# Optimization experiments

Hardware: AMD Instinct MI355X
Metric: run time of the kernel (lower is better)

## Reference

```python
import jax, jax.numpy as jnp
import numpy as np

N_NODES = 10000
N_EDGES = 640000
D = 128


def _sage_conv(x, src, dst, W_l, b, W_r):
    # PyG SAGEConv (mean aggr): out = lin_l(mean_{j in N(i)} x_j) + lin_r(x_i)
    msgs = x[src]                                        # [E, D_in] gather
    agg = jax.ops.segment_sum(msgs, dst, num_segments=N_NODES)  # [N, D_in]
    deg = jax.ops.segment_sum(jnp.ones((src.shape[0],), x.dtype), dst,
                              num_segments=N_NODES)
    agg = agg / jnp.maximum(deg, 1.0)[:, None]           # mean; isolated nodes -> 0
    return agg @ W_l + b + x @ W_r


def setup_inputs() -> dict:
    key = jax.random.key(0)
    ks = jax.random.split(key, 8)
    s = 1.0 / np.sqrt(D)
    return {
        "x": jax.random.normal(ks[0], (N_NODES, D), dtype=jnp.float32),
        "edge_index": jax.random.randint(ks[1], (2, N_EDGES), 0, N_NODES, dtype=jnp.int64),
        "W_l0": jax.random.normal(ks[2], (D, D), dtype=jnp.float32) * s,
        "b0": jnp.zeros((D,), dtype=jnp.float32),
        "W_r0": jax.random.normal(ks[3], (D, D), dtype=jnp.float32) * s,
        "W_l1": jax.random.normal(ks[4], (D, D), dtype=jnp.float32) * s,
        "b1": jnp.zeros((D,), dtype=jnp.float32),
        "W_r1": jax.random.normal(ks[5], (D, D), dtype=jnp.float32) * s,
    }


def reference(x, edge_index, W_l0, b0, W_r0, W_l1, b1, W_r1):
    # Dropout(p=0.3) is identity in eval mode (reference runs inference math).
    src, dst = edge_index[0], edge_index[1]
    h = jax.nn.elu(_sage_conv(x, src, dst, W_l0, b0, W_r0))
    h = jax.nn.elu(_sage_conv(h, src, dst, W_l1, b1, W_r1))
    return h
```

## Files before the change

kernel.cpp:

```cpp
#include <hip/hip_runtime.h>

#define N_NODES 10000
#define N_EDGES 640000
#define D 128
#define MAXDEG 128
#define NBUCK 157
#define BCAP 6144
#define EPT 10

typedef unsigned int uint;
typedef unsigned short u16;
typedef short bf16x8 __attribute__((ext_vector_type(8)));
typedef float f32x4 __attribute__((ext_vector_type(4)));

__device__ __forceinline__ u16 f2bf(float f) {
    uint u = __float_as_uint(f);
    return (u16)((u + 0x7fffu + ((u >> 16) & 1u)) >> 16);
}
__device__ __forceinline__ float bflo(uint v) { return __uint_as_float(v << 16); }
__device__ __forceinline__ float bfhi(uint v) { return __uint_as_float(v & 0xffff0000u); }

__global__ void detect_kernel(const void* ei, int* flag) {
    const int* p = (const int*)ei;
    bool nz = false;
    for (int it = 0; it < 16; ++it) {
        int i = 2 * (threadIdx.x + it * 256) + 1;
        if (p[i] != 0) nz = true;
    }
    if (__any(nz) && (threadIdx.x & 63) == 0) flag[0] = 1;
}

__device__ __forceinline__ int edge_at(const void* ei, int is32, int idx) {
    if (is32) return ((const int*)ei)[idx];
    return (int)((const long long*)ei)[idx];
}

__global__ __launch_bounds__(256)
void binp1_kernel(const void* __restrict__ ei, const int* __restrict__ flag,
                  int* __restrict__ gcount, uint* __restrict__ gbucket) {
    __shared__ int hist[NBUCK];
    __shared__ int base[NBUCK];
    const int t = threadIdx.x;
    if (t < NBUCK) hist[t] = 0;
    __syncthreads();
    const int is32 = *flag;
    const int e0 = blockIdx.x * (256 * EPT);
    uint pk[EPT];
    int  rk[EPT];
#pragma unroll
    for (int i = 0; i < EPT; ++i) {
        int e  = e0 + i * 256 + t;
        int s  = edge_at(ei, is32, e);
        int dn = edge_at(ei, is32, N_EDGES + e);
        pk[i] = ((uint)dn << 16) | (uint)s;
        rk[i] = atomicAdd(&hist[dn >> 6], 1);
    }
    __syncthreads();
    if (t < NBUCK) base[t] = atomicAdd(&gcount[t], hist[t]);
    __syncthreads();
#pragma unroll
    for (int i = 0; i < EPT; ++i) {
        int bkt = (int)(pk[i] >> 22);
        int pos = base[bkt] + rk[i];
        if (pos < BCAP) gbucket[(size_t)bkt * BCAP + pos] = pk[i];
    }
}

__global__ __launch_bounds__(256)
void binp2_kernel(const int* __restrict__ gcount, const uint* __restrict__ gbucket,
                  u16* __restrict__ adj, int* __restrict__ deg_g) {
    __shared__ __align__(16) u16 tile[64][MAXDEG];
    __shared__ int cur[64];
    const int b = blockIdx.x;
    const int t = threadIdx.x;
    if (t < 64) cur[t] = 0;
    __syncthreads();
    const int total = min(gcount[b], BCAP);
    for (int e = t; e < total; e += 256) {
        uint pk = gbucket[(size_t)b * BCAP + e];
        int ln  = (int)((pk >> 16) & 63u);
        int src = (int)(pk & 0xffffu);
        int r = atomicAdd(&cur[ln], 1);
        if (r < MAXDEG) tile[ln][r] = (u16)src;
    }
    __syncthreads();
    const int node0 = b * 64;
    if (t < 64 && node0 + t < N_NODES) deg_g[node0 + t] = cur[t];
    const uint4* ts = (const uint4*)&tile[0][0];
#pragma unroll
    for (int q = 0; q < 4; ++q) {
        int i = t + q * 256;
        int node = node0 + (i >> 4);
        if (node < N_NODES) ((uint4*)(adj + (size_t)node * MAXDEG))[i & 15] = ts[i];
    }
}

__global__ void cast_kernel(const float* __restrict__ in, uint* __restrict__ outb) {
    int t = blockIdx.x * 256 + threadIdx.x;
    if (t >= N_NODES * D / 8) return;
    const float4* p = (const float4*)in + (size_t)t * 2;
    float4 a = p[0], b = p[1];
    uint4 r;
    r.x = (uint)f2bf(a.x) | ((uint)f2bf(a.y) << 16);
    r.y = (uint)f2bf(a.z) | ((uint)f2bf(a.w) << 16);
    r.z = (uint)f2bf(b.x) | ((uint)f2bf(b.y) << 16);
    r.w = (uint)f2bf(b.z) | ((uint)f2bf(b.w) << 16);
    ((uint4*)outb)[t] = r;
}

__global__ __launch_bounds__(256)
void wprep_kernel(const float* __restrict__ Wl0, const float* __restrict__ Wr0,
                  const float* __restrict__ Wl1, const float* __restrict__ Wr1,
                  u16* __restrict__ WT0, u16* __restrict__ WT1) {
    const int b = blockIdx.x;
    const int layer = b >> 7, d = b & 127, k = threadIdx.x;
    const float* Wl = layer ? Wl1 : Wl0;
    const float* Wr = layer ? Wr1 : Wr0;
    u16* WT = layer ? WT1 : WT0;
    float v = (k < 128) ? Wl[k * D + d] : Wr[(k - 128) * D + d];
    WT[(size_t)d * 256 + k] = f2bf(v);
}

__global__ __launch_bounds__(256)
void gather_kernel(const uint* __restrict__ xb2, const u16* __restrict__ adj,
                   const int* __restrict__ deg_g, uint* __restrict__ aggb2) {
    const int node = blockIdx.x * 4 + (threadIdx.x >> 6);
    const int lane = threadIdx.x & 63;
    const int dg = deg_g[node];
    const int cnt = min(dg, MAXDEG);
    const uint* __restrict__ rowu = (const uint*)(adj + (size_t)node * MAXDEG);
    float a0 = 0.f, a1 = 0.f;
    const int nb16 = cnt >> 4;
    if (nb16 > 0) {
        uint pkb[8];
#pragma unroll
        for (int i = 0; i < 8; ++i) pkb[i] = rowu[i];
        for (int b = 0; b < nb16; ++b) {
            uint cur[8];
#pragma unroll
            for (int i = 0; i < 8; ++i) cur[i] = pkb[i];
            if (b + 1 < nb16) {
#pragma unroll
                for (int i = 0; i < 8; ++i) pkb[i] = rowu[(b + 1) * 8 + i];
            }
            uint v[16];
#pragma unroll
            for (int i = 0; i < 8; ++i) {
                v[2 * i]     = xb2[(size_t)(cur[i] & 0xffffu) * 64 + lane];
                v[2 * i + 1] = xb2[(size_t)(cur[i] >> 16)     * 64 + lane];
            }
#pragma unroll
            for (int i = 0; i < 16; ++i) { a0 += bflo(v[i]); a1 += bfhi(v[i]); }
        }
    }
    for (int p = nb16 << 4; p < cnt; ++p) {
        uint v = xb2[(size_t)((const u16*)rowu)[p] * 64 + lane];
        a0 += bflo(v);
        a1 += bfhi(v);
    }
    float inv = 1.0f / fmaxf((float)dg, 1.0f);
    aggb2[(size_t)node * 64 + lane] = (uint)f2bf(a0 * inv) | ((uint)f2bf(a1 * inv) << 16);
}

__global__ __launch_bounds__(256)
void mfma_gemm_kernel(const uint* __restrict__ aggb2, const uint* __restrict__ xb2,
                      const u16* __restrict__ WT, const float* __restrict__ bias,
                      float* __restrict__ outf ,
                      u16* __restrict__ outb ) {
    __shared__ __align__(16) u16 A_lds[16 * 256];
    const int t = threadIdx.x;
    const int nb = blockIdx.x * 16;
    {
        const int row = t >> 4, c = t & 15;
        const int node = nb + row;
        uint4 va = ((const uint4*)(aggb2 + (size_t)node * 64))[c];
        uint4 vx = ((const uint4*)(xb2  + (size_t)node * 64))[c];
        char* base = (char*)A_lds + row * 512;
        const int swz = (row & 7) << 4;
        *(uint4*)(base + ((c * 16) ^ swz))       = va;
        *(uint4*)(base + ((256 + c * 16) ^ swz)) = vx;
    }
    __syncthreads();

    const int w = t >> 6, l = t & 63;
    const int lr = l & 15, g = l >> 4;
    f32x4 acc0 = {0.f, 0.f, 0.f, 0.f}, acc1 = {0.f, 0.f, 0.f, 0.f};
    const char* abase = (const char*)A_lds + lr * 512;
    const int aswz = (lr & 7) << 4;
    const u16* wt0 = WT + (size_t)(w * 32 + lr) * 256;
    const u16* wt1 = WT + (size_t)(w * 32 + 16 + lr) * 256;
#pragma unroll
    for (int kk = 0; kk < 8; ++kk) {
        bf16x8 af  = *(const bf16x8*)(abase + ((kk * 64 + g * 16) ^ aswz));
        bf16x8 bf0 = *(const bf16x8*)(wt0 + kk * 32 + g * 8);
        bf16x8 bf1 = *(const bf16x8*)(wt1 + kk * 32 + g * 8);
        acc0 = __builtin_amdgcn_mfma_f32_16x16x32_bf16(af, bf0, acc0, 0, 0, 0);
        acc1 = __builtin_amdgcn_mfma_f32_16x16x32_bf16(af, bf1, acc1, 0, 0, 0);
    }

    const int col0 = w * 32 + lr, col1 = col0 + 16;
    const float b0v = bias[col0], b1v = bias[col1];
#pragma unroll
    for (int j = 0; j < 4; ++j) {
        const int node = nb + g * 4 + j;
        float v0 = acc0[j] + b0v; v0 = v0 > 0.f ? v0 : expm1f(v0);
        float v1 = acc1[j] + b1v; v1 = v1 > 0.f ? v1 : expm1f(v1);
        if (outf) {
            outf[(size_t)node * D + col0] = v0;
            outf[(size_t)node * D + col1] = v1;
        }
        if (outb) {
            outb[(size_t)node * D + col0] = f2bf(v0);
            outb[(size_t)node * D + col1] = f2bf(v1);
        }
    }
}

extern "C" void kernel_launch(void* const* d_in, const int* in_sizes, int n_in,
                              void* d_out, int out_size, void* d_ws, size_t ws_size,
                              hipStream_t stream) {
    const float* x   = (const float*)d_in[0];
    const void*  ei  = d_in[1];
    const float* Wl0 = (const float*)d_in[2];
    const float* b0  = (const float*)d_in[3];
    const float* Wr0 = (const float*)d_in[4];
    const float* Wl1 = (const float*)d_in[5];
    const float* b1  = (const float*)d_in[6];
    const float* Wr1 = (const float*)d_in[7];
    float* out = (float*)d_out;

    char* ws = (char*)d_ws;
    int*  flag    = (int*)(ws + 0);
    int*  gcount  = (int*)(ws + 1024);
    int*  deg     = (int*)(ws + 4096);
    u16*  adj     = (u16*)(ws + 65536);
    uint* gbucket = (uint*)(ws + 3145728);
    uint* xb2     = (uint*)(ws + 3145728);
    uint* yb2     = (uint*)(ws + 5767168);
    uint* aggb2   = (uint*)(ws + 8388608);
    u16*  WT0     = (u16*)(ws + 11010048);
    u16*  WT1     = (u16*)(ws + 11075584);

    hipMemsetAsync(ws, 0, 2048, stream);

    detect_kernel<<<1, 256, 0, stream>>>(ei, flag);
    binp1_kernel<<<250, 256, 0, stream>>>(ei, flag, gcount, gbucket);
    binp2_kernel<<<NBUCK, 256, 0, stream>>>(gcount, gbucket, adj, deg);
    cast_kernel<<<625, 256, 0, stream>>>(x, xb2);
    wprep_kernel<<<256, 256, 0, stream>>>(Wl0, Wr0, Wl1, Wr1, WT0, WT1);

    gather_kernel<<<2500, 256, 0, stream>>>(xb2, adj, deg, aggb2);
    mfma_gemm_kernel<<<625, 256, 0, stream>>>(aggb2, xb2, WT0, b0, (float*)0, (u16*)yb2);

    gather_kernel<<<2500, 256, 0, stream>>>(yb2, adj, deg, aggb2);
    mfma_gemm_kernel<<<625, 256, 0, stream>>>(aggb2, yb2, WT1, b1, out, (u16*)0);
}
```

Measured before the change: 85.97 us.

## Vectorize neighbor gather with zero-row padding and merge preprocessing launches

The gather kernel now splits each wave into four 16-lane groups. Each group loads a full 256-byte neighbor row with uint4 loads, so four neighbors are processed at once, and the partial sums are combined with cross-lane shuffles. Adjacency rows are padded with a dedicated zero row (ZROW), zeroed in both the x and y buffers, which removes the scalar tail loop. The separate detect, binning-phase-2, cast and weight-prep launches are folded: index-width detection moves into each binp1 block, and the other three stages become one multi-role prep kernel. This cuts launch count and gives wider memory transactions, at the cost of reading padded entries, extra shuffles, and relying on per-block width detection.

```diff
diff --git a/kernel.cpp b/kernel.cpp
--- a/kernel.cpp
+++ b/kernel.cpp
@@ -6,7 +6,8 @@
 #define MAXDEG 128
 #define NBUCK 157
 #define BCAP 6144
-#define EPT 10
+#define EPT 5
+#define ZROW 10000
 
 typedef unsigned int uint;
 typedef unsigned short u16;
@@ -20,31 +21,25 @@
 __device__ __forceinline__ float bflo(uint v) { return __uint_as_float(v << 16); }
 __device__ __forceinline__ float bfhi(uint v) { return __uint_as_float(v & 0xffff0000u); }
 
-__global__ void detect_kernel(const void* ei, int* flag) {
-    const int* p = (const int*)ei;
-    bool nz = false;
-    for (int it = 0; it < 16; ++it) {
-        int i = 2 * (threadIdx.x + it * 256) + 1;
-        if (p[i] != 0) nz = true;
-    }
-    if (__any(nz) && (threadIdx.x & 63) == 0) flag[0] = 1;
-}
-
 __device__ __forceinline__ int edge_at(const void* ei, int is32, int idx) {
     if (is32) return ((const int*)ei)[idx];
     return (int)((const long long*)ei)[idx];
 }
 
 __global__ __launch_bounds__(256)
-void binp1_kernel(const void* __restrict__ ei, const int* __restrict__ flag,
-                  int* __restrict__ gcount, uint* __restrict__ gbucket) {
+void binp1_kernel(const void* __restrict__ ei, int* __restrict__ gcount,
+                  uint* __restrict__ gbucket) {
     __shared__ int hist[NBUCK];
     __shared__ int base[NBUCK];
+    __shared__ int s_is32;
     const int t = threadIdx.x;
     if (t < NBUCK) hist[t] = 0;
-    __syncthreads();
-    const int is32 = *flag;
+    if (t == 0) s_is32 = 0;
+    __syncthreads();
     const int e0 = blockIdx.x * (256 * EPT);
+    if (((const int*)ei)[2 * (e0 + t) + 1] != 0) s_is32 = 1;
+    __syncthreads();
+    const int is32 = s_is32;
     uint pk[EPT];
     int  rk[EPT];
 #pragma unroll
@@ -67,99 +62,119 @@
 }
 
 __global__ __launch_bounds__(256)
-void binp2_kernel(const int* __restrict__ gcount, const uint* __restrict__ gbucket,
-                  u16* __restrict__ adj, int* __restrict__ deg_g) {
+void prep_kernel(const int* __restrict__ gcount, const uint* __restrict__ gbucket,
+                 u16* __restrict__ adj, int* __restrict__ deg_g,
+                 const float* __restrict__ x, uint* __restrict__ xb2,
+                 const float* __restrict__ Wl0, const float* __restrict__ Wr0,
+                 const float* __restrict__ Wl1, const float* __restrict__ Wr1,
+                 u16* __restrict__ WT0, u16* __restrict__ WT1) {
+    const int b = blockIdx.x;
+    const int t = threadIdx.x;
     __shared__ __align__(16) u16 tile[64][MAXDEG];
     __shared__ int cur[64];
-    const int b = blockIdx.x;
-    const int t = threadIdx.x;
-    if (t < 64) cur[t] = 0;
-    __syncthreads();
-    const int total = min(gcount[b], BCAP);
-    for (int e = t; e < total; e += 256) {
-        uint pk = gbucket[(size_t)b * BCAP + e];
-        int ln  = (int)((pk >> 16) & 63u);
-        int src = (int)(pk & 0xffffu);
-        int r = atomicAdd(&cur[ln], 1);
-        if (r < MAXDEG) tile[ln][r] = (u16)src;
-    }
-    __syncthreads();
-    const int node0 = b * 64;
-    if (t < 64 && node0 + t < N_NODES) deg_g[node0 + t] = cur[t];
-    const uint4* ts = (const uint4*)&tile[0][0];
-#pragma unroll
-    for (int q = 0; q < 4; ++q) {
-        int i = t + q * 256;
-        int node = node0 + (i >> 4);
-        if (node < N_NODES) ((uint4*)(adj + (size_t)node * MAXDEG))[i & 15] = ts[i];
-    }
-}
-
-__global__ void cast_kernel(const float* __restrict__ in, uint* __restrict__ outb) {
-    int t = blockIdx.x * 256 + threadIdx.x;
-    if (t >= N_NODES * D / 8) return;
-    const float4* p = (const float4*)in + (size_t)t * 2;
-    float4 a = p[0], b = p[1];
-    uint4 r;
-    r.x = (uint)f2bf(a.x) | ((uint)f2bf(a.y) << 16);
-    r.y = (uint)f2bf(a.z) | ((uint)f2bf(a.w) << 16);
-    r.z = (uint)f2bf(b.x) | ((uint)f2bf(b.y) << 16);
-    r.w = (uint)f2bf(b.z) | ((uint)f2bf(b.w) << 16);
-    ((uint4*)outb)[t] = r;
-}
-
-__global__ __launch_bounds__(256)
-void wprep_kernel(const float* __restrict__ Wl0, const float* __restrict__ Wr0,
-                  const float* __restrict__ Wl1, const float* __restrict__ Wr1,
-                  u16* __restrict__ WT0, u16* __restrict__ WT1) {
-    const int b = blockIdx.x;
-    const int layer = b >> 7, d = b & 127, k = threadIdx.x;
-    const float* Wl = layer ? Wl1 : Wl0;
-    const float* Wr = layer ? Wr1 : Wr0;
-    u16* WT = layer ? WT1 : WT0;
-    float v = (k < 128) ? Wl[k * D + d] : Wr[(k - 128) * D + d];
-    WT[(size_t)d * 256 + k] = f2bf(v);
+    if (b < NBUCK) {
+        uint* tw = (uint*)&tile[0][0];
+#pragma unroll
+        for (int q = 0; q < 16; ++q) tw[t + q * 256] = ((uint)ZROW << 16) | ZROW;
+        if (t < 64) cur[t] = 0;
+        __syncthreads();
+        const int total = min(gcount[b], BCAP);
+        for (int e = t; e < total; e += 256) {
+            uint pk = gbucket[(size_t)b * BCAP + e];
+            int ln = (int)((pk >> 16) & 63u);
+            int r = atomicAdd(&cur[ln], 1);
+            if (r < MAXDEG) tile[ln][r] = (u16)(pk & 0xffffu);
+        }
+        __syncthreads();
+        const int node0 = b * 64;
+        if (t < 64 && node0 + t < N_NODES) deg_g[node0 + t] = cur[t];
+        const uint4* ts = (const uint4*)&tile[0][0];
+#pragma unroll
+        for (int q = 0; q < 4; ++q) {
+            int i = t + q * 256;
+            int node = node0 + (i >> 4);
+            if (node < N_NODES) ((uint4*)(adj + (size_t)node * MAXDEG))[i & 15] = ts[i];
+        }
+    } else if (b < NBUCK + 625) {
+        int idx = (b - NBUCK) * 256 + t;
+        const float4* p = (const float4*)x + (size_t)idx * 2;
+        float4 a = p[0], bb = p[1];
+        uint4 r;
+        r.x = (uint)f2bf(a.x) | ((uint)f2bf(a.y) << 16);
+        r.y = (uint)f2bf(a.z) | ((uint)f2bf(a.w) << 16);
+        r.z = (uint)f2bf(bb.x) | ((uint)f2bf(bb.y) << 16);
+        r.w = (uint)f2bf(bb.z) | ((uint)f2bf(bb.w) << 16);
+        ((uint4*)xb2)[idx] = r;
+    } else if (b < NBUCK + 625 + 256) {
+        int b2 = b - (NBUCK + 625);
+        int layer = b2 >> 7, d = b2 & 127, k = t;
+        const float* Wl = layer ? Wl1 : Wl0;
+        const float* Wr = layer ? Wr1 : Wr0;
+        u16* WT = layer ? WT1 : WT0;
+        float v = (k < 128) ? Wl[k * D + d] : Wr[(k - 128) * D + d];
+        WT[(size_t)d * 256 + k] = f2bf(v);
+    } else {
+        if (t < 16) ((uint4*)(xb2 + (size_t)ZROW * 64))[t] = make_uint4(0, 0, 0, 0);
+    }
 }
 
 __global__ __launch_bounds__(256)
 void gather_kernel(const uint* __restrict__ xb2, const u16* __restrict__ adj,
                    const int* __restrict__ deg_g, uint* __restrict__ aggb2) {
     const int node = blockIdx.x * 4 + (threadIdx.x >> 6);
-    const int lane = threadIdx.x & 63;
+    const int l = threadIdx.x & 63;
+    const int g = l >> 4;
+    const int c = l & 15;
+    const int half = g >> 1;
+    const int sh = (g & 1) << 4;
     const int dg = deg_g[node];
     const int cnt = min(dg, MAXDEG);
-    const uint* __restrict__ rowu = (const uint*)(adj + (size_t)node * MAXDEG);
-    float a0 = 0.f, a1 = 0.f;
-    const int nb16 = cnt >> 4;
-    if (nb16 > 0) {
-        uint pkb[8];
-#pragma unroll
-        for (int i = 0; i < 8; ++i) pkb[i] = rowu[i];
-        for (int b = 0; b < nb16; ++b) {
-            uint cur[8];
-#pragma unroll
-            for (int i = 0; i < 8; ++i) cur[i] = pkb[i];
-            if (b + 1 < nb16) {
-#pragma unroll
-                for (int i = 0; i < 8; ++i) pkb[i] = rowu[(b + 1) * 8 + i];
-            }
-            uint v[16];
-#pragma unroll
-            for (int i = 0; i < 8; ++i) {
-                v[2 * i]     = xb2[(size_t)(cur[i] & 0xffffu) * 64 + lane];
-                v[2 * i + 1] = xb2[(size_t)(cur[i] >> 16)     * 64 + lane];
-            }
-#pragma unroll
-            for (int i = 0; i < 16; ++i) { a0 += bflo(v[i]); a1 += bfhi(v[i]); }
-        }
-    }
-    for (int p = nb16 << 4; p < cnt; ++p) {
-        uint v = xb2[(size_t)((const u16*)rowu)[p] * 64 + lane];
-        a0 += bflo(v);
-        a1 += bfhi(v);
-    }
-    float inv = 1.0f / fmaxf((float)dg, 1.0f);
-    aggb2[(size_t)node * 64 + lane] = (uint)f2bf(a0 * inv) | ((uint)f2bf(a1 * inv) << 16);
+    const uint4* __restrict__ rowq = (const uint4*)(adj + (size_t)node * MAXDEG);
+    float acc[8];
+#pragma unroll
+    for (int i = 0; i < 8; ++i) acc[i] = 0.f;
+    const int nch = (cnt + 15) >> 4;
+#pragma unroll 2
+    for (int ch = 0; ch < nch; ++ch) {
+        uint4 wa = rowq[2 * ch];
+        uint4 wb = rowq[2 * ch + 1];
+        uint a0 = half ? wa.y : wa.x;
+        uint a1 = half ? wa.w : wa.z;
+        uint b0 = half ? wb.y : wb.x;
+        uint b1 = half ? wb.w : wb.z;
+        uint id0 = (a0 >> sh) & 0xffffu;
+        uint id1 = (a1 >> sh) & 0xffffu;
+        uint id2 = (b0 >> sh) & 0xffffu;
+        uint id3 = (b1 >> sh) & 0xffffu;
+        uint4 v0 = ((const uint4*)(xb2 + (size_t)id0 * 64))[c];
+        uint4 v1 = ((const uint4*)(xb2 + (size_t)id1 * 64))[c];
+        uint4 v2 = ((const uint4*)(xb2 + (size_t)id2 * 64))[c];
+        uint4 v3 = ((const uint4*)(xb2 + (size_t)id3 * 64))[c];
+        acc[0] += bflo(v0.x) + bflo(v1.x) + bflo(v2.x) + bflo(v3.x);
+        acc[1] += bfhi(v0.x) + bfhi(v1.x) + bfhi(v2.x) + bfhi(v3.x);
+        acc[2] += bflo(v0.y) + bflo(v1.y) + bflo(v2.y) + bflo(v3.y);
+        acc[3] += bfhi(v0.y) + bfhi(v1.y) + bfhi(v2.y) + bfhi(v3.y);
+        acc[4] += bflo(v0.z) + bflo(v1.z) + bflo(v2.z) + bflo(v3.z);
+        acc[5] += bfhi(v0.z) + bfhi(v1.z) + bfhi(v2.z) + bfhi(v3.z);
+        acc[6] += bflo(v0.w) + bflo(v1.w) + bflo(v2.w) + bflo(v3.w);
+        acc[7] += bfhi(v0.w) + bfhi(v1.w) + bfhi(v2.w) + bfhi(v3.w);
+    }
+#pragma unroll
+    for (int i = 0; i < 8; ++i) {
+        float r = acc[i];
+        r += __shfl_xor(r, 16, 64);
+        r += __shfl_xor(r, 32, 64);
+        acc[i] = r;
+    }
+    if (g == 0) {
+        float inv = 1.0f / fmaxf((float)dg, 1.0f);
+        uint4 o;
+        o.x = (uint)f2bf(acc[0] * inv) | ((uint)f2bf(acc[1] * inv) << 16);
+        o.y = (uint)f2bf(acc[2] * inv) | ((uint)f2bf(acc[3] * inv) << 16);
+        o.z = (uint)f2bf(acc[4] * inv) | ((uint)f2bf(acc[5] * inv) << 16);
+        o.w = (uint)f2bf(acc[6] * inv) | ((uint)f2bf(acc[7] * inv) << 16);
+        ((uint4*)(aggb2 + (size_t)node * 64))[c] = o;
+    }
 }
 
 __global__ __launch_bounds__(256)
@@ -214,6 +229,8 @@
             outb[(size_t)node * D + col1] = f2bf(v1);
         }
     }
+    if (outb && blockIdx.x == 0 && t < 16)
+        ((uint4*)(outb + (size_t)ZROW * D))[t] = make_uint4(0, 0, 0, 0);
 }
 
 extern "C" void kernel_launch(void* const* d_in, const int* in_sizes, int n_in,
@@ -230,24 +247,21 @@
     float* out = (float*)d_out;
 
     char* ws = (char*)d_ws;
-    int*  flag    = (int*)(ws + 0);
     int*  gcount  = (int*)(ws + 1024);
     int*  deg     = (int*)(ws + 4096);
     u16*  adj     = (u16*)(ws + 65536);
     uint* gbucket = (uint*)(ws + 3145728);
-    uint* xb2     = (uint*)(ws + 3145728);
-    uint* yb2     = (uint*)(ws + 5767168);
-    uint* aggb2   = (uint*)(ws + 8388608);
-    u16*  WT0     = (u16*)(ws + 11010048);
-    u16*  WT1     = (u16*)(ws + 11075584);
-
-    hipMemsetAsync(ws, 0, 2048, stream);
-
-    detect_kernel<<<1, 256, 0, stream>>>(ei, flag);
-    binp1_kernel<<<250, 256, 0, stream>>>(ei, flag, gcount, gbucket);
-    binp2_kernel<<<NBUCK, 256, 0, stream>>>(gcount, gbucket, adj, deg);
-    cast_kernel<<<625, 256, 0, stream>>>(x, xb2);
-    wprep_kernel<<<256, 256, 0, stream>>>(Wl0, Wr0, Wl1, Wr1, WT0, WT1);
+    uint* yb2     = (uint*)(ws + 3145728);
+    uint* aggb2   = (uint*)(ws + 5705984);
+    uint* xb2     = (uint*)(ws + 8266240);
+    u16*  WT0     = (u16*)(ws + 10826752);
+    u16*  WT1     = (u16*)(ws + 10892288);
+
+    hipMemsetAsync(ws, 0, 4096, stream);
+
+    binp1_kernel<<<500, 256, 0, stream>>>(ei, gcount, gbucket);
+    prep_kernel<<<NBUCK + 625 + 256 + 1, 256, 0, stream>>>(
+        gcount, gbucket, adj, deg, x, xb2, Wl0, Wr0, Wl1, Wr1, WT0, WT1);
 
     gather_kernel<<<2500, 256, 0, stream>>>(xb2, adj, deg, aggb2);
     mfma_gemm_kernel<<<625, 256, 0, stream>>>(aggb2, xb2, WT0, b0, (float*)0, (u16*)yb2);
```

Result: faster. 79.84 us (-7.1%).
